# Optimization experiments

Hardware: AMD Instinct MI355X
Metric: run time of the kernel (lower is better)

## Reference

```python
import jax, jax.numpy as jnp
import numpy as np

DIM = 256
HEADS = 8
B, T, D, H, W = 2, 8, 16, 16, 16


def _mha(x, wqkv, bqkv, wo, bo):
    # x: [M, S, F]; standard self-attention (q=k=v=x), LoRA rank 0.
    M, S, F = x.shape
    hd = F // HEADS
    qkv = jnp.einsum('msf,kfg->kmsg', x, wqkv) + bqkv[:, None, None, :]  # [3,M,S,F]
    q, k, v = qkv
    q = q.reshape(M, S, HEADS, hd).transpose(0, 2, 1, 3)  # [M,Hh,S,hd]
    k = k.reshape(M, S, HEADS, hd).transpose(0, 2, 1, 3)
    v = v.reshape(M, S, HEADS, hd).transpose(0, 2, 1, 3)
    scores = jnp.einsum('mhsd,mhtd->mhst', q, k) / jnp.sqrt(jnp.asarray(hd, x.dtype))
    attn = jax.nn.softmax(scores, axis=-1)
    out = jnp.einsum('mhst,mhtd->mhsd', attn, v)
    out = out.transpose(0, 2, 1, 3).reshape(M, S, F)
    return out @ wo + bo


def _make_params(key, name_suffix):
    k1, k2 = jax.random.split(key)
    s = 1.0 / np.sqrt(DIM)
    return {
        f'wqkv_{name_suffix}': jax.random.normal(k1, (3, DIM, DIM), jnp.float32) * s,
        f'bqkv_{name_suffix}': jnp.zeros((3, DIM), jnp.float32),
        f'wo_{name_suffix}': jax.random.normal(k2, (DIM, DIM), jnp.float32) * s,
        f'bo_{name_suffix}': jnp.zeros((DIM,), jnp.float32),
    }


def setup_inputs() -> dict:
    key = jax.random.key(0)
    ks = jax.random.split(key, 5)
    inp = {'x': jax.random.normal(ks[0], (B, T, D * H * W, DIM), jnp.float32)}
    for k, ax in zip(ks[1:], ['t', 'd', 'h', 'w']):
        inp.update(_make_params(k, ax))
    inp['grid_d'] = D
    inp['grid_h'] = H
    inp['grid_w'] = W
    return inp


def reference(x, wqkv_t, bqkv_t, wo_t, bo_t,
              wqkv_d, bqkv_d, wo_d, bo_d,
              wqkv_h, bqkv_h, wo_h, bo_h,
              wqkv_w, bqkv_w, wo_w, bo_w,
              grid_d, grid_h, grid_w):
    b, t, n, f = x.shape
    d, h, w = grid_d, grid_h, grid_w
    x = x.reshape(b, t, d, h, w, f)
    if t > 1:
        xt = x.transpose(0, 2, 3, 4, 1, 5).reshape(b * d * h * w, t, f)
        xt = _mha(xt, wqkv_t, bqkv_t, wo_t, bo_t)
        xt = xt.reshape(b, d, h, w, t, f).transpose(0, 4, 1, 2, 3, 5)
        x = x + xt
    xd = x.transpose(0, 1, 3, 4, 2, 5).reshape(b * t * h * w, d, f)
    xd = _mha(xd, wqkv_d, bqkv_d, wo_d, bo_d)
    xd = xd.reshape(b, t, h, w, d, f).transpose(0, 1, 4, 2, 3, 5)
    xh = x.transpose(0, 1, 2, 4, 3, 5).reshape(b * t * d * w, h, f)
    xh = _mha(xh, wqkv_h, bqkv_h, wo_h, bo_h)
    xh = xh.reshape(b, t, d, w, h, f).transpose(0, 1, 2, 4, 3, 5)
    xw = x.reshape(b * t * d * h, w, f)
    xw = _mha(xw, wqkv_w, bqkv_w, wo_w, bo_w)
    xw = xw.reshape(b, t, d, h, w, f)
    x_comb = x + xd + xh + xw
    return x_comb.reshape(b, t, d * h * w, f)
```

## Files before the change

### kernel.cpp

```cpp
#include <hip/hip_runtime.h>

typedef __attribute__((ext_vector_type(4))) float f32x4;
typedef __attribute__((ext_vector_type(8))) short s16x8;

__device__ __forceinline__ ushort f2bf(float f) {
  union { float f; uint u; } v; v.f = f;
  uint r = v.u + 0x7fffu + ((v.u >> 16) & 1u);
  return (ushort)(r >> 16);
}

__device__ __forceinline__ void glds16(const void* g, void* l) {
  __builtin_amdgcn_global_load_lds(
      (const __attribute__((address_space(1))) uint*)g,
      (__attribute__((address_space(3))) uint*)l, 16, 0, 0);
}

__device__ __forceinline__ int asidx(int row, int col) {
  return row*256 + ((((col>>3) ^ ((row&7)<<2)))<<3) + (col&7);
}
__device__ __forceinline__ int scridx(int row, int col) {
  return row*32 + ((((col>>3) ^ ((row>>2)&3)))<<3) + (col&7);
}

struct WSrc { const float* p[8]; };

__global__ __launch_bounds__(256) void prep_weights(WSrc s, ushort* wq, ushort* wo) {
  int mm = blockIdx.x >> 6;
  int t  = blockIdx.x & 63;
  int a = mm >> 2, sub = mm & 3;
  const float* src = (sub < 3) ? (s.p[a*2] + sub*65536) : s.p[a*2+1];
  ushort*      dst = (sub < 3) ? (wq + (a*3 + sub)*65536) : (wo + a*65536);
  int gt = (t >> 3) * 32, ft = (t & 7) * 32;
  __shared__ float tile[32][33];
  int lx = threadIdx.x & 31, ly = threadIdx.x >> 5;
#pragma unroll
  for (int i = 0; i < 4; i++)
    tile[ly + i*8][lx] = src[(ft + ly + i*8)*256 + gt + lx];
  __syncthreads();
#pragma unroll
  for (int i = 0; i < 4; i++) {
    int n = gt + ly + i*8, col = ft + lx;
    dst[asidx(n, col)] = f2bf(tile[lx][ly + i*8]);
  }
}

template<int AXIS>
__device__ __forceinline__ int token_index(int blk, int row) {
  if (AXIS == 0) {
    int seq = blk*8 + (row >> 3);
    int t = row & 7;
    int b = seq >> 12, n = seq & 4095;
    return (b*8 + t)*4096 + n;
  } else {
    int sid = blk*4 + (row >> 4);
    int bt = sid >> 8, lo = sid & 255, r = row & 15;
    if (AXIS == 1) { int hh = lo >> 4, ww = lo & 15; return bt*4096 + r*256 + hh*16 + ww; }
    if (AXIS == 2) { int dd = lo >> 4, ww = lo & 15; return bt*4096 + dd*256 + r*16 + ww; }
    { int dd = lo >> 4, hh = lo & 15; return bt*4096 + dd*256 + hh*16 + r; }
  }
}

#define PUB_BARRIER() do { \
    __builtin_amdgcn_sched_barrier(0); \
    asm volatile("s_waitcnt lgkmcnt(0)" ::: "memory"); \
    __builtin_amdgcn_sched_barrier(0); \
    __builtin_amdgcn_s_barrier(); \
    __builtin_amdgcn_sched_barrier(0); } while (0)

template<int AXIS>
__global__ __launch_bounds__(512, 4) void axial_pass(
    const float* __restrict__ x0, const ushort* __restrict__ xb,
    const ushort* __restrict__ wqkvT, const float* __restrict__ bqkv,
    const ushort* __restrict__ woT, const float* __restrict__ bo,
    float* __restrict__ out, ushort* __restrict__ x1b) {

  __shared__ ushort Wbuf[2][8192];
  __shared__ ushort As[16384];
  __shared__ ushort Scr[4][2048];

  const int tid = threadIdx.x, blk = blockIdx.x;
  const int wv = tid >> 6, lane = tid & 63, llo = lane & 15, lhi = lane >> 4;
  const int pr = wv >> 1, half = wv & 1;
  const int rr = half*16 + llo;
  ushort* Qs = Scr[pr];
  ushort* Ks = Qs + 512;
  ushort* Vt = Qs + 1024;
  const f32x4 fzero = {0.f, 0.f, 0.f, 0.f};
  const s16x8 szero = {0,0,0,0,0,0,0,0};

  auto issue_stage = [&](int s) {
    const ushort* src = (s < 24) ? (wqkvT + (s % 3)*65536 + (s / 3)*8192)
                                 : (woT + (s - 24)*8192);
    const ushort* g = src + wv*1024 + lane*8;
    ushort* l = &Wbuf[s & 1][wv*1024];
    glds16(g, l);
    glds16(g + 512, l + 512);
  };

#define STAGE_SYNC(sn) do { \
    __builtin_amdgcn_sched_barrier(0); \
    asm volatile("s_waitcnt vmcnt(0) lgkmcnt(0)" ::: "memory"); \
    __builtin_amdgcn_sched_barrier(0); \
    __builtin_amdgcn_s_barrier(); \
    __builtin_amdgcn_sched_barrier(0); \
    if ((sn) < 32) issue_stage(sn); \
  } while (0)

  issue_stage(0);

  {
    int row = tid >> 3, j = tid & 7;
    int tok = token_index<AXIS>(blk, row);
    if (AXIS == 0) {
      const float4* s4 = (const float4*)(x0 + (size_t)tok*256);
#pragma unroll
      for (int i = 0; i < 4; i++) {
        int c = j + 8*i;
        float4 v0 = s4[c*2], v1 = s4[c*2 + 1];
        s16x8 o;
        o[0] = (short)f2bf(v0.x); o[1] = (short)f2bf(v0.y);
        o[2] = (short)f2bf(v0.z); o[3] = (short)f2bf(v0.w);
        o[4] = (short)f2bf(v1.x); o[5] = (short)f2bf(v1.y);
        o[6] = (short)f2bf(v1.z); o[7] = (short)f2bf(v1.w);
        *(s16x8*)(As + asidx(row, c*8)) = o;
      }
    } else {
      const s16x8* s8 = (const s16x8*)(xb + (size_t)tok*256);
#pragma unroll
      for (int i = 0; i < 4; i++) {
        int c = j + 8*i;
        *(s16x8*)(As + asidx(row, c*8)) = s8[c];
      }
    }
  }
  {
    int row = half*16 + (lane >> 2);
    int cc = 2 + (lane & 1);
    *(s16x8*)(Vt + row*32 + ((cc ^ ((row>>2)&3))<<3)) = szero;
  }
  __syncthreads();

  s16x8 af[8];
  const int xrow = pr*16 + llo;
#pragma unroll
  for (int ks = 0; ks < 8; ks++)
    af[ks] = *(const s16x8*)(As + asidx(xrow, (ks*4 + lhi)*8));

  auto proj = [&](int sb) -> f32x4 {
    const ushort* buf = Wbuf[sb];
    f32x4 c = fzero;
#pragma unroll
    for (int ks = 0; ks < 8; ks++) {
      s16x8 bv = *(const s16x8*)(buf + rr*256 + ((((ks*4+lhi) ^ ((rr&7)<<2)))<<3));
      c = __builtin_amdgcn_mfma_f32_16x16x32_bf16(af[ks], bv, c, 0, 0, 0);
    }
    return c;
  };

#pragma unroll 1
  for (int h = 0; h < 8; h++) {
    STAGE_SYNC(3*h + 1);
    {
      f32x4 c = proj((3*h) & 1);
      float bias = bqkv[0*256 + h*32 + rr];
#pragma unroll
      for (int r = 0; r < 4; r++)
        Qs[scridx(lhi*4 + r, rr)] = f2bf(c[r] + bias);
    }
    STAGE_SYNC(3*h + 2);
    {
      f32x4 c = proj((3*h + 1) & 1);
      float bias = bqkv[1*256 + h*32 + rr];
#pragma unroll
      for (int r = 0; r < 4; r++)
        Ks[scridx(lhi*4 + r, rr)] = f2bf(c[r] + bias);
    }
    STAGE_SYNC(3*h + 3);
    {
      f32x4 c = proj((3*h + 2) & 1);
      float bias = bqkv[2*256 + h*32 + rr];
#pragma unroll
      for (int r = 0; r < 4; r++)
        Vt[scridx(rr, lhi*4 + r)] = f2bf(c[r] + bias);

      s16x8 aq = *(const s16x8*)(Qs + scridx(llo, lhi*8));
      s16x8 bk = *(const s16x8*)(Ks + scridx(llo, lhi*8));
      f32x4 sc = __builtin_amdgcn_mfma_f32_16x16x32_bf16(aq, bk, fzero, 0, 0, 0);

      PUB_BARRIER();

#pragma unroll
      for (int r = 0; r < 4; r++) {
        float s = sc[r] * 0.17677669529663689f;
        if (AXIS == 0) {
          int srow = lhi*4 + r;
          if ((srow >> 3) != (llo >> 3)) s = -1e30f;
        }
        float mx = s;
        mx = fmaxf(mx, __shfl_xor(mx, 1));
        mx = fmaxf(mx, __shfl_xor(mx, 2));
        mx = fmaxf(mx, __shfl_xor(mx, 4));
        mx = fmaxf(mx, __shfl_xor(mx, 8));
        float e = __expf(s - mx);
        float sm = e;
        sm += __shfl_xor(sm, 1);
        sm += __shfl_xor(sm, 2);
        sm += __shfl_xor(sm, 4);
        sm += __shfl_xor(sm, 8);
        Ks[scridx(lhi*4 + r, llo)] = f2bf(e * __builtin_amdgcn_rcpf(sm));
      }
      s16x8 ap = *(const s16x8*)(Ks + scridx(llo, lhi*8));
      s16x8 bv = *(const s16x8*)(Vt + scridx(rr, lhi*8));
      f32x4 o = __builtin_amdgcn_mfma_f32_16x16x32_bf16(ap, bv, fzero, 0, 0, 0);
#pragma unroll
      for (int r = 0; r < 4; r++)
        As[asidx(pr*16 + lhi*4 + r, h*32 + rr)] = f2bf(o[r]);
    }
  }

  f32x4 acc[8];
#pragma unroll 1
  for (int st = 0; st < 8; st++) {
    STAGE_SYNC(25 + st);
    if (st == 0) {
#pragma unroll
      for (int ks = 0; ks < 8; ks++)
        af[ks] = *(const s16x8*)(As + asidx(xrow, (ks*4 + lhi)*8));
#pragma unroll
      for (int i = 0; i < 8; i++) acc[i] = fzero;
    }
    {
      const ushort* buf = Wbuf[st & 1];
#pragma unroll
      for (int ks = 0; ks < 8; ks++) {
        s16x8 bw = *(const s16x8*)(buf + rr*256 + ((((ks*4+lhi) ^ ((rr&7)<<2)))<<3));
        acc[st] = __builtin_amdgcn_mfma_f32_16x16x32_bf16(af[ks], bw, acc[st], 0, 0, 0);
      }
    }
  }

#pragma unroll
  for (int r = 0; r < 4; r++) {
    int row = pr*16 + lhi*4 + r;
    int tok = token_index<AXIS>(blk, row);
    size_t base = (size_t)tok*256;
#pragma unroll
    for (int st = 0; st < 8; st++) {
      int f = st*32 + half*16 + llo;
      float v = acc[st][r] + bo[f];
      if (AXIS == 0) {
        v += x0[base + f];
        out[base + f] = v;
        x1b[base + f] = f2bf(v);
      } else {
        out[base + f] += v;
      }
    }
  }
#undef STAGE_SYNC
}

extern "C" void kernel_launch(void* const* d_in, const int* in_sizes, int n_in,
                              void* d_out, int out_size, void* d_ws, size_t ws_size,
                              hipStream_t stream) {
  const float* x = (const float*)d_in[0];
  ushort* wq  = (ushort*)d_ws;
  ushort* wo  = wq + 4*3*65536;
  ushort* x1b = wo + 4*65536;
  float* out = (float*)d_out;

  WSrc wsrc;
  wsrc.p[0] = (const float*)d_in[1];  wsrc.p[1] = (const float*)d_in[3];
  wsrc.p[2] = (const float*)d_in[5];  wsrc.p[3] = (const float*)d_in[7];
  wsrc.p[4] = (const float*)d_in[9];  wsrc.p[5] = (const float*)d_in[11];
  wsrc.p[6] = (const float*)d_in[13]; wsrc.p[7] = (const float*)d_in[15];
  prep_weights<<<dim3(1024), dim3(256), 0, stream>>>(wsrc, wq, wo);

  const float* bq_t = (const float*)d_in[2];  const float* bo_t = (const float*)d_in[4];
  const float* bq_d = (const float*)d_in[6];  const float* bo_d = (const float*)d_in[8];
  const float* bq_h = (const float*)d_in[10]; const float* bo_h = (const float*)d_in[12];
  const float* bq_w = (const float*)d_in[14]; const float* bo_w = (const float*)d_in[16];

  axial_pass<0><<<dim3(1024), dim3(512), 0, stream>>>(x, nullptr, wq + 0*3*65536, bq_t, wo + 0*65536, bo_t, out, x1b);
  axial_pass<1><<<dim3(1024), dim3(512), 0, stream>>>(nullptr, x1b, wq + 1*3*65536, bq_d, wo + 1*65536, bo_d, out, nullptr);
  axial_pass<2><<<dim3(1024), dim3(512), 0, stream>>>(nullptr, x1b, wq + 2*3*65536, bq_h, wo + 2*65536, bo_h, out, nullptr);
  axial_pass<3><<<dim3(1024), dim3(512), 0, stream>>>(nullptr, x1b, wq + 3*3*65536, bq_w, wo + 3*65536, bo_w, out, nullptr);
}
```

Before: 435.8 us.

## Stage epilogue through LDS for float4 stores; split MFMA chains and change swizzle

The output epilogue now writes accumulators to a swizzled fp32 LDS tile, then each thread reads contiguous float4 chunks and does vectorized global load/add/store with bias, instead of scattered scalar accesses. The projection MFMA loops are split into two independent accumulation chains, with setprio raised around them. The As/W swizzle is changed to XOR by row&7. Shared buffers are merged into one array so the epilogue can reuse the weight region. This adds two barriers and an extra LDS round trip.

```diff
diff --git a/kernel.cpp b/kernel.cpp
--- a/kernel.cpp
+++ b/kernel.cpp
@@ -16,10 +16,13 @@
 }
 
 __device__ __forceinline__ int asidx(int row, int col) {
-  return row*256 + ((((col>>3) ^ ((row&7)<<2)))<<3) + (col&7);
+  return row*256 + ((((col>>3) ^ (row & 7)))<<3) + (col&7);
 }
 __device__ __forceinline__ int scridx(int row, int col) {
   return row*32 + ((((col>>3) ^ ((row>>2)&3)))<<3) + (col&7);
+}
+__device__ __forceinline__ int epidx(int row, int f) {
+  return row*256 + (f ^ ((row & 7) << 2));
 }
 
 struct WSrc { const float* p[8]; };
@@ -74,15 +77,17 @@
     const ushort* __restrict__ woT, const float* __restrict__ bo,
     float* __restrict__ out, ushort* __restrict__ x1b) {
 
-  __shared__ ushort Wbuf[2][8192];
-  __shared__ ushort As[16384];
-  __shared__ ushort Scr[4][2048];
+  __shared__ ushort smem[40960];
+  ushort* Wb0 = smem;
+  ushort* Wb1 = smem + 8192;
+  ushort* As  = smem + 16384;
+  ushort* ScrB = smem + 32768;
 
   const int tid = threadIdx.x, blk = blockIdx.x;
   const int wv = tid >> 6, lane = tid & 63, llo = lane & 15, lhi = lane >> 4;
   const int pr = wv >> 1, half = wv & 1;
   const int rr = half*16 + llo;
-  ushort* Qs = Scr[pr];
+  ushort* Qs = ScrB + pr*2048;
   ushort* Ks = Qs + 512;
   ushort* Vt = Qs + 1024;
   const f32x4 fzero = {0.f, 0.f, 0.f, 0.f};
@@ -92,7 +97,7 @@
     const ushort* src = (s < 24) ? (wqkvT + (s % 3)*65536 + (s / 3)*8192)
                                  : (woT + (s - 24)*8192);
     const ushort* g = src + wv*1024 + lane*8;
-    ushort* l = &Wbuf[s & 1][wv*1024];
+    ushort* l = ((s & 1) ? Wb1 : Wb0) + wv*1024;
     glds16(g, l);
     glds16(g + 512, l + 512);
   };
@@ -147,14 +152,18 @@
     af[ks] = *(const s16x8*)(As + asidx(xrow, (ks*4 + lhi)*8));
 
   auto proj = [&](int sb) -> f32x4 {
-    const ushort* buf = Wbuf[sb];
-    f32x4 c = fzero;
-#pragma unroll
-    for (int ks = 0; ks < 8; ks++) {
-      s16x8 bv = *(const s16x8*)(buf + rr*256 + ((((ks*4+lhi) ^ ((rr&7)<<2)))<<3));
-      c = __builtin_amdgcn_mfma_f32_16x16x32_bf16(af[ks], bv, c, 0, 0, 0);
-    }
-    return c;
+    const ushort* buf = sb ? Wb1 : Wb0;
+    f32x4 ca = fzero, cb = fzero;
+    __builtin_amdgcn_s_setprio(1);
+#pragma unroll
+    for (int ks = 0; ks < 4; ks++) {
+      s16x8 b0 = *(const s16x8*)(buf + asidx(rr, (ks*4 + lhi)*8));
+      s16x8 b1 = *(const s16x8*)(buf + asidx(rr, ((ks+4)*4 + lhi)*8));
+      ca = __builtin_amdgcn_mfma_f32_16x16x32_bf16(af[ks],   b0, ca, 0, 0, 0);
+      cb = __builtin_amdgcn_mfma_f32_16x16x32_bf16(af[ks+4], b1, cb, 0, 0, 0);
+    }
+    __builtin_amdgcn_s_setprio(0);
+    return ca + cb;
   };
 
 #pragma unroll 1
@@ -230,30 +239,53 @@
       for (int i = 0; i < 8; i++) acc[i] = fzero;
     }
     {
-      const ushort* buf = Wbuf[st & 1];
-#pragma unroll
-      for (int ks = 0; ks < 8; ks++) {
-        s16x8 bw = *(const s16x8*)(buf + rr*256 + ((((ks*4+lhi) ^ ((rr&7)<<2)))<<3));
-        acc[st] = __builtin_amdgcn_mfma_f32_16x16x32_bf16(af[ks], bw, acc[st], 0, 0, 0);
-      }
-    }
-  }
-
-#pragma unroll
-  for (int r = 0; r < 4; r++) {
-    int row = pr*16 + lhi*4 + r;
+      const ushort* buf = (st & 1) ? Wb1 : Wb0;
+      f32x4 t0 = fzero;
+      __builtin_amdgcn_s_setprio(1);
+#pragma unroll
+      for (int ks = 0; ks < 4; ks++) {
+        s16x8 b0 = *(const s16x8*)(buf + asidx(rr, (ks*4 + lhi)*8));
+        s16x8 b1 = *(const s16x8*)(buf + asidx(rr, ((ks+4)*4 + lhi)*8));
+        acc[st] = __builtin_amdgcn_mfma_f32_16x16x32_bf16(af[ks],   b0, acc[st], 0, 0, 0);
+        t0      = __builtin_amdgcn_mfma_f32_16x16x32_bf16(af[ks+4], b1, t0,      0, 0, 0);
+      }
+      __builtin_amdgcn_s_setprio(0);
+      acc[st] = acc[st] + t0;
+    }
+  }
+
+  float* Fep = (float*)smem;
+  PUB_BARRIER();
+#pragma unroll
+  for (int st = 0; st < 8; st++) {
+#pragma unroll
+    for (int r = 0; r < 4; r++) {
+      int row = pr*16 + lhi*4 + r;
+      Fep[epidx(row, st*32 + half*16 + llo)] = acc[st][r];
+    }
+  }
+  PUB_BARRIER();
+  {
+    int row = tid >> 3, g = tid & 7;
     int tok = token_index<AXIS>(blk, row);
     size_t base = (size_t)tok*256;
 #pragma unroll
-    for (int st = 0; st < 8; st++) {
-      int f = st*32 + half*16 + llo;
-      float v = acc[st][r] + bo[f];
+    for (int i = 0; i < 8; i++) {
+      int f = i*32 + g*4;
+      float4 v = *(float4*)&Fep[epidx(row, f)];
+      float4 b = *(const float4*)&bo[f];
+      v.x += b.x; v.y += b.y; v.z += b.z; v.w += b.w;
       if (AXIS == 0) {
-        v += x0[base + f];
-        out[base + f] = v;
-        x1b[base + f] = f2bf(v);
+        float4 x = *(const float4*)&x0[base + f];
+        v.x += x.x; v.y += x.y; v.z += x.z; v.w += x.w;
+        *(float4*)&out[base + f] = v;
+        ushort4 p; p.x = f2bf(v.x); p.y = f2bf(v.y);
+        p.z = f2bf(v.z); p.w = f2bf(v.w);
+        *(ushort4*)&x1b[base + f] = p;
       } else {
-        out[base + f] += v;
+        float4 o = *(float4*)&out[base + f];
+        o.x += v.x; o.y += v.y; o.z += v.z; o.w += v.w;
+        *(float4*)&out[base + f] = o;
       }
     }
   }
```

After: 402.8 us. 7.6% less time.

## Double rows per block and keep activations in registers across projections

Applied to the files above, without the earlier changes.

Each block now processes 128 token rows instead of 64, halving the grid, so each staged weight tile loaded into LDS feeds twice as many MFMAs. Input activations and per-head attention outputs are loaded straight into registers instead of going through a shared A tile. The epilogue stages accumulators through LDS so global reads and writes become float4-vectorised rather than scalar. It also adds s_setprio around the MFMA loops and fully unrolls the head loop, which raises register pressure and may reduce occupancy.

```diff
diff --git a/kernel.cpp b/kernel.cpp
--- a/kernel.cpp
+++ b/kernel.cpp
@@ -16,10 +16,13 @@
 }
 
 __device__ __forceinline__ int asidx(int row, int col) {
-  return row*256 + ((((col>>3) ^ ((row&7)<<2)))<<3) + (col&7);
+  return row*256 + ((((col>>3) ^ (row & 7)))<<3) + (col&7);
 }
 __device__ __forceinline__ int scridx(int row, int col) {
   return row*32 + ((((col>>3) ^ ((row>>2)&3)))<<3) + (col&7);
+}
+__device__ __forceinline__ int scrfidx(int row, int c) {
+  return row*32 + (c ^ ((row & 7) << 2));
 }
 
 struct WSrc { const float* p[8]; };
@@ -47,16 +50,16 @@
 template<int AXIS>
 __device__ __forceinline__ int token_index(int blk, int row) {
   if (AXIS == 0) {
-    int seq = blk*8 + (row >> 3);
+    int seq = blk*16 + (row >> 3);
     int t = row & 7;
     int b = seq >> 12, n = seq & 4095;
     return (b*8 + t)*4096 + n;
   } else {
-    int sid = blk*4 + (row >> 4);
+    int sid = blk*8 + (row >> 4);
     int bt = sid >> 8, lo = sid & 255, r = row & 15;
-    if (AXIS == 1) { int hh = lo >> 4, ww = lo & 15; return bt*4096 + r*256 + hh*16 + ww; }
+    if (AXIS == 1) return bt*4096 + r*256 + lo;
     if (AXIS == 2) { int dd = lo >> 4, ww = lo & 15; return bt*4096 + dd*256 + r*16 + ww; }
-    { int dd = lo >> 4, hh = lo & 15; return bt*4096 + dd*256 + hh*16 + r; }
+    return bt*4096 + lo*16 + r;
   }
 }
 
@@ -74,25 +77,22 @@
     const ushort* __restrict__ woT, const float* __restrict__ bo,
     float* __restrict__ out, ushort* __restrict__ x1b) {
 
-  __shared__ ushort Wbuf[2][8192];
-  __shared__ ushort As[16384];
-  __shared__ ushort Scr[4][2048];
+  __shared__ ushort smem[28672];
+  ushort* Wb0 = smem;
+  ushort* Wb1 = smem + 8192;
+  ushort* QKP = smem + 16384;
+  ushort* Vt  = smem + 24576;
 
   const int tid = threadIdx.x, blk = blockIdx.x;
   const int wv = tid >> 6, lane = tid & 63, llo = lane & 15, lhi = lane >> 4;
-  const int pr = wv >> 1, half = wv & 1;
-  const int rr = half*16 + llo;
-  ushort* Qs = Scr[pr];
-  ushort* Ks = Qs + 512;
-  ushort* Vt = Qs + 1024;
+  const int rg = wv >> 1, ch = wv & 1;
   const f32x4 fzero = {0.f, 0.f, 0.f, 0.f};
-  const s16x8 szero = {0,0,0,0,0,0,0,0};
 
   auto issue_stage = [&](int s) {
     const ushort* src = (s < 24) ? (wqkvT + (s % 3)*65536 + (s / 3)*8192)
                                  : (woT + (s - 24)*8192);
     const ushort* g = src + wv*1024 + lane*8;
-    ushort* l = &Wbuf[s & 1][wv*1024];
+    ushort* l = ((s & 1) ? Wb1 : Wb0) + wv*1024;
     glds16(g, l);
     glds16(g + 512, l + 512);
   };
@@ -108,152 +108,195 @@
 
   issue_stage(0);
 
-  {
-    int row = tid >> 3, j = tid & 7;
+  s16x8 af[2][8];
+#pragma unroll
+  for (int g = 0; g < 2; g++) {
+    int row = rg*32 + g*16 + llo;
     int tok = token_index<AXIS>(blk, row);
     if (AXIS == 0) {
-      const float4* s4 = (const float4*)(x0 + (size_t)tok*256);
-#pragma unroll
-      for (int i = 0; i < 4; i++) {
-        int c = j + 8*i;
-        float4 v0 = s4[c*2], v1 = s4[c*2 + 1];
+      const float* xp = x0 + (size_t)tok*256;
+#pragma unroll
+      for (int ks = 0; ks < 8; ks++) {
+        float4 a = *(const float4*)(xp + ks*32 + lhi*8);
+        float4 b = *(const float4*)(xp + ks*32 + lhi*8 + 4);
         s16x8 o;
-        o[0] = (short)f2bf(v0.x); o[1] = (short)f2bf(v0.y);
-        o[2] = (short)f2bf(v0.z); o[3] = (short)f2bf(v0.w);
-        o[4] = (short)f2bf(v1.x); o[5] = (short)f2bf(v1.y);
-        o[6] = (short)f2bf(v1.z); o[7] = (short)f2bf(v1.w);
-        *(s16x8*)(As + asidx(row, c*8)) = o;
+        o[0] = (short)f2bf(a.x); o[1] = (short)f2bf(a.y);
+        o[2] = (short)f2bf(a.z); o[3] = (short)f2bf(a.w);
+        o[4] = (short)f2bf(b.x); o[5] = (short)f2bf(b.y);
+        o[6] = (short)f2bf(b.z); o[7] = (short)f2bf(b.w);
+        af[g][ks] = o;
       }
     } else {
-      const s16x8* s8 = (const s16x8*)(xb + (size_t)tok*256);
-#pragma unroll
-      for (int i = 0; i < 4; i++) {
-        int c = j + 8*i;
-        *(s16x8*)(As + asidx(row, c*8)) = s8[c];
-      }
-    }
-  }
-  {
-    int row = half*16 + (lane >> 2);
-    int cc = 2 + (lane & 1);
-    *(s16x8*)(Vt + row*32 + ((cc ^ ((row>>2)&3))<<3)) = szero;
-  }
-  __syncthreads();
-
-  s16x8 af[8];
-  const int xrow = pr*16 + llo;
-#pragma unroll
-  for (int ks = 0; ks < 8; ks++)
-    af[ks] = *(const s16x8*)(As + asidx(xrow, (ks*4 + lhi)*8));
-
-  auto proj = [&](int sb) -> f32x4 {
-    const ushort* buf = Wbuf[sb];
-    f32x4 c = fzero;
-#pragma unroll
-    for (int ks = 0; ks < 8; ks++) {
-      s16x8 bv = *(const s16x8*)(buf + rr*256 + ((((ks*4+lhi) ^ ((rr&7)<<2)))<<3));
-      c = __builtin_amdgcn_mfma_f32_16x16x32_bf16(af[ks], bv, c, 0, 0, 0);
-    }
-    return c;
-  };
-
-#pragma unroll 1
+      const ushort* xp = xb + (size_t)tok*256;
+#pragma unroll
+      for (int ks = 0; ks < 8; ks++)
+        af[g][ks] = *(const s16x8*)(xp + ks*32 + lhi*8);
+    }
+  }
+
+  s16x8 af_o[8];
+
+#pragma unroll
   for (int h = 0; h < 8; h++) {
     STAGE_SYNC(3*h + 1);
     {
-      f32x4 c = proj((3*h) & 1);
-      float bias = bqkv[0*256 + h*32 + rr];
-#pragma unroll
-      for (int r = 0; r < 4; r++)
-        Qs[scridx(lhi*4 + r, rr)] = f2bf(c[r] + bias);
+      const ushort* buf = ((3*h) & 1) ? Wb1 : Wb0;
+      f32x4 c0 = fzero, c1 = fzero;
+      __builtin_amdgcn_s_setprio(1);
+#pragma unroll
+      for (int ks = 0; ks < 8; ks++) {
+        s16x8 bv = *(const s16x8*)(buf + asidx(ch*16 + llo, (ks*4 + lhi)*8));
+        c0 = __builtin_amdgcn_mfma_f32_16x16x32_bf16(af[0][ks], bv, c0, 0, 0, 0);
+        c1 = __builtin_amdgcn_mfma_f32_16x16x32_bf16(af[1][ks], bv, c1, 0, 0, 0);
+      }
+      __builtin_amdgcn_s_setprio(0);
+      float bi = bqkv[h*32 + ch*16 + llo];
+      ushort* q0 = QKP + (rg*2 + 0)*1024;
+      ushort* q1 = QKP + (rg*2 + 1)*1024;
+#pragma unroll
+      for (int r = 0; r < 4; r++) {
+        q0[scridx(lhi*4 + r, ch*16 + llo)] = f2bf(c0[r] + bi);
+        q1[scridx(lhi*4 + r, ch*16 + llo)] = f2bf(c1[r] + bi);
+      }
     }
     STAGE_SYNC(3*h + 2);
     {
-      f32x4 c = proj((3*h + 1) & 1);
-      float bias = bqkv[1*256 + h*32 + rr];
-#pragma unroll
-      for (int r = 0; r < 4; r++)
-        Ks[scridx(lhi*4 + r, rr)] = f2bf(c[r] + bias);
+      const ushort* buf = ((3*h + 1) & 1) ? Wb1 : Wb0;
+      f32x4 c0 = fzero, c1 = fzero;
+      __builtin_amdgcn_s_setprio(1);
+#pragma unroll
+      for (int ks = 0; ks < 8; ks++) {
+        s16x8 bv = *(const s16x8*)(buf + asidx(ch*16 + llo, (ks*4 + lhi)*8));
+        c0 = __builtin_amdgcn_mfma_f32_16x16x32_bf16(af[0][ks], bv, c0, 0, 0, 0);
+        c1 = __builtin_amdgcn_mfma_f32_16x16x32_bf16(af[1][ks], bv, c1, 0, 0, 0);
+      }
+      __builtin_amdgcn_s_setprio(0);
+      float bi = bqkv[256 + h*32 + ch*16 + llo];
+      ushort* k0 = QKP + (rg*2 + 0)*1024 + 512;
+      ushort* k1 = QKP + (rg*2 + 1)*1024 + 512;
+#pragma unroll
+      for (int r = 0; r < 4; r++) {
+        k0[scridx(lhi*4 + r, ch*16 + llo)] = f2bf(c0[r] + bi);
+        k1[scridx(lhi*4 + r, ch*16 + llo)] = f2bf(c1[r] + bi);
+      }
     }
     STAGE_SYNC(3*h + 3);
     {
-      f32x4 c = proj((3*h + 2) & 1);
-      float bias = bqkv[2*256 + h*32 + rr];
-#pragma unroll
-      for (int r = 0; r < 4; r++)
-        Vt[scridx(rr, lhi*4 + r)] = f2bf(c[r] + bias);
-
-      s16x8 aq = *(const s16x8*)(Qs + scridx(llo, lhi*8));
-      s16x8 bk = *(const s16x8*)(Ks + scridx(llo, lhi*8));
+      const ushort* buf = ((3*h + 2) & 1) ? Wb1 : Wb0;
+      f32x4 c0 = fzero, c1 = fzero;
+      __builtin_amdgcn_s_setprio(1);
+#pragma unroll
+      for (int ks = 0; ks < 8; ks++) {
+        s16x8 bv = *(const s16x8*)(buf + asidx(ch*16 + llo, (ks*4 + lhi)*8));
+        c0 = __builtin_amdgcn_mfma_f32_16x16x32_bf16(af[0][ks], bv, c0, 0, 0, 0);
+        c1 = __builtin_amdgcn_mfma_f32_16x16x32_bf16(af[1][ks], bv, c1, 0, 0, 0);
+      }
+      __builtin_amdgcn_s_setprio(0);
+      float bi = bqkv[512 + h*32 + ch*16 + llo];
+      ushort* vt = Vt + rg*1024;
+#pragma unroll
+      for (int r = 0; r < 4; r++) {
+        vt[scridx(ch*16 + llo, 0*16 + lhi*4 + r)] = f2bf(c0[r] + bi);
+        vt[scridx(ch*16 + llo, 1*16 + lhi*4 + r)] = f2bf(c1[r] + bi);
+      }
+    }
+    PUB_BARRIER();
+
+    {
+      ushort* myQ  = QKP + wv*1024;
+      ushort* myKP = myQ + 512;
+      const ushort* myVt = Vt + (wv >> 1)*1024;
+      const int mh = wv & 1;
+      s16x8 aq = *(const s16x8*)(myQ  + scridx(llo, lhi*8));
+      s16x8 bk = *(const s16x8*)(myKP + scridx(llo, lhi*8));
       f32x4 sc = __builtin_amdgcn_mfma_f32_16x16x32_bf16(aq, bk, fzero, 0, 0, 0);
-
-      PUB_BARRIER();
-
-#pragma unroll
-      for (int r = 0; r < 4; r++) {
-        float s = sc[r] * 0.17677669529663689f;
+#pragma unroll
+      for (int r = 0; r < 4; r++) {
+        float sv = sc[r] * 0.17677669529663689f;
         if (AXIS == 0) {
           int srow = lhi*4 + r;
-          if ((srow >> 3) != (llo >> 3)) s = -1e30f;
+          if ((srow >> 3) != (llo >> 3)) sv = -1e30f;
         }
-        float mx = s;
+        float mx = sv;
         mx = fmaxf(mx, __shfl_xor(mx, 1));
         mx = fmaxf(mx, __shfl_xor(mx, 2));
         mx = fmaxf(mx, __shfl_xor(mx, 4));
         mx = fmaxf(mx, __shfl_xor(mx, 8));
-        float e = __expf(s - mx);
+        float e = __expf(sv - mx);
         float sm = e;
         sm += __shfl_xor(sm, 1);
         sm += __shfl_xor(sm, 2);
         sm += __shfl_xor(sm, 4);
         sm += __shfl_xor(sm, 8);
-        Ks[scridx(lhi*4 + r, llo)] = f2bf(e * __builtin_amdgcn_rcpf(sm));
-      }
-      s16x8 ap = *(const s16x8*)(Ks + scridx(llo, lhi*8));
-      s16x8 bv = *(const s16x8*)(Vt + scridx(rr, lhi*8));
-      f32x4 o = __builtin_amdgcn_mfma_f32_16x16x32_bf16(ap, bv, fzero, 0, 0, 0);
-#pragma unroll
-      for (int r = 0; r < 4; r++)
-        As[asidx(pr*16 + lhi*4 + r, h*32 + rr)] = f2bf(o[r]);
-    }
-  }
-
-  f32x4 acc[8];
+        myKP[scridx(lhi*4 + r, mh*16 + llo)]       = f2bf(e * __builtin_amdgcn_rcpf(sm));
+        myKP[scridx(lhi*4 + r, (1 - mh)*16 + llo)] = 0;
+      }
+      s16x8 ap  = *(const s16x8*)(myKP + scridx(llo, lhi*8));
+      s16x8 bv0 = *(const s16x8*)(myVt + scridx(llo, lhi*8));
+      s16x8 bv1 = *(const s16x8*)(myVt + scridx(16 + llo, lhi*8));
+      f32x4 o0 = __builtin_amdgcn_mfma_f32_16x16x32_bf16(ap, bv0, fzero, 0, 0, 0);
+      f32x4 o1 = __builtin_amdgcn_mfma_f32_16x16x32_bf16(ap, bv1, fzero, 0, 0, 0);
+#pragma unroll
+      for (int r = 0; r < 4; r++) {
+        myQ[scridx(lhi*4 + r, llo)]      = f2bf(o0[r]);
+        myQ[scridx(lhi*4 + r, 16 + llo)] = f2bf(o1[r]);
+      }
+      af_o[h] = *(const s16x8*)(myQ + scridx(llo, lhi*8));
+    }
+  }
+
 #pragma unroll 1
   for (int st = 0; st < 8; st++) {
     STAGE_SYNC(25 + st);
-    if (st == 0) {
-#pragma unroll
-      for (int ks = 0; ks < 8; ks++)
-        af[ks] = *(const s16x8*)(As + asidx(xrow, (ks*4 + lhi)*8));
-#pragma unroll
-      for (int i = 0; i < 8; i++) acc[i] = fzero;
-    }
-    {
-      const ushort* buf = Wbuf[st & 1];
-#pragma unroll
-      for (int ks = 0; ks < 8; ks++) {
-        s16x8 bw = *(const s16x8*)(buf + rr*256 + ((((ks*4+lhi) ^ ((rr&7)<<2)))<<3));
-        acc[st] = __builtin_amdgcn_mfma_f32_16x16x32_bf16(af[ks], bw, acc[st], 0, 0, 0);
-      }
-    }
-  }
-
-#pragma unroll
-  for (int r = 0; r < 4; r++) {
-    int row = pr*16 + lhi*4 + r;
-    int tok = token_index<AXIS>(blk, row);
-    size_t base = (size_t)tok*256;
-#pragma unroll
-    for (int st = 0; st < 8; st++) {
-      int f = st*32 + half*16 + llo;
-      float v = acc[st][r] + bo[f];
+    const ushort* buf = (st & 1) ? Wb1 : Wb0;
+    f32x4 c0 = fzero, c1 = fzero;
+    __builtin_amdgcn_s_setprio(1);
+#pragma unroll
+    for (int ks = 0; ks < 8; ks++) {
+      s16x8 b0 = *(const s16x8*)(buf + asidx(llo,      (ks*4 + lhi)*8));
+      s16x8 b1 = *(const s16x8*)(buf + asidx(16 + llo, (ks*4 + lhi)*8));
+      c0 = __builtin_amdgcn_mfma_f32_16x16x32_bf16(af_o[ks], b0, c0, 0, 0, 0);
+      c1 = __builtin_amdgcn_mfma_f32_16x16x32_bf16(af_o[ks], b1, c1, 0, 0, 0);
+    }
+    __builtin_amdgcn_s_setprio(0);
+
+    float* Scf = (float*)(QKP + wv*1024);
+#pragma unroll
+    for (int r = 0; r < 4; r++) {
+      Scf[scrfidx(lhi*4 + r, llo)]      = c0[r];
+      Scf[scrfidx(lhi*4 + r, 16 + llo)] = c1[r];
+    }
+    {
+      int row = lane >> 2, cb = (lane & 3)*8;
+      float4 fa = *(const float4*)&Scf[scrfidx(row, cb)];
+      float4 fb = *(const float4*)&Scf[scrfidx(row, cb + 4)];
+      int col = st*32 + cb;
+      int tok = token_index<AXIS>(blk, wv*16 + row);
+      size_t base = (size_t)tok*256;
+      float4 ba = *(const float4*)&bo[col];
+      float4 bb4 = *(const float4*)&bo[col + 4];
+      fa.x += ba.x; fa.y += ba.y; fa.z += ba.z; fa.w += ba.w;
+      fb.x += bb4.x; fb.y += bb4.y; fb.z += bb4.z; fb.w += bb4.w;
       if (AXIS == 0) {
-        v += x0[base + f];
-        out[base + f] = v;
-        x1b[base + f] = f2bf(v);
+        float4 xa = *(const float4*)&x0[base + col];
+        float4 xb4 = *(const float4*)&x0[base + col + 4];
+        fa.x += xa.x; fa.y += xa.y; fa.z += xa.z; fa.w += xa.w;
+        fb.x += xb4.x; fb.y += xb4.y; fb.z += xb4.z; fb.w += xb4.w;
+        *(float4*)&out[base + col]     = fa;
+        *(float4*)&out[base + col + 4] = fb;
+        s16x8 p;
+        p[0] = (short)f2bf(fa.x); p[1] = (short)f2bf(fa.y);
+        p[2] = (short)f2bf(fa.z); p[3] = (short)f2bf(fa.w);
+        p[4] = (short)f2bf(fb.x); p[5] = (short)f2bf(fb.y);
+        p[6] = (short)f2bf(fb.z); p[7] = (short)f2bf(fb.w);
+        *(s16x8*)&x1b[base + col] = p;
       } else {
-        out[base + f] += v;
+        float4 oa = *(float4*)&out[base + col];
+        float4 ob = *(float4*)&out[base + col + 4];
+        oa.x += fa.x; oa.y += fa.y; oa.z += fa.z; oa.w += fa.w;
+        ob.x += fb.x; ob.y += fb.y; ob.z += fb.z; ob.w += fb.w;
+        *(float4*)&out[base + col]     = oa;
+        *(float4*)&out[base + col + 4] = ob;
       }
     }
   }
@@ -281,8 +324,8 @@
   const float* bq_h = (const float*)d_in[10]; const float* bo_h = (const float*)d_in[12];
   const float* bq_w = (const float*)d_in[14]; const float* bo_w = (const float*)d_in[16];
 
-  axial_pass<0><<<dim3(1024), dim3(512), 0, stream>>>(x, nullptr, wq + 0*3*65536, bq_t, wo + 0*65536, bo_t, out, x1b);
-  axial_pass<1><<<dim3(1024), dim3(512), 0, stream>>>(nullptr, x1b, wq + 1*3*65536, bq_d, wo + 1*65536, bo_d, out, nullptr);
-  axial_pass<2><<<dim3(1024), dim3(512), 0, stream>>>(nullptr, x1b, wq + 2*3*65536, bq_h, wo + 2*65536, bo_h, out, nullptr);
-  axial_pass<3><<<dim3(1024), dim3(512), 0, stream>>>(nullptr, x1b, wq + 3*3*65536, bq_w, wo + 3*65536, bo_w, out, nullptr);
-}
+  axial_pass<0><<<dim3(512), dim3(512), 0, stream>>>(x, nullptr, wq + 0*3*65536, bq_t, wo + 0*65536, bo_t, out, x1b);
+  axial_pass<1><<<dim3(512), dim3(512), 0, stream>>>(nullptr, x1b, wq + 1*3*65536, bq_d, wo + 1*65536, bo_d, out, nullptr);
+  axial_pass<2><<<dim3(512), dim3(512), 0, stream>>>(nullptr, x1b, wq + 2*3*65536, bq_h, wo + 2*65536, bo_h, out, nullptr);
+  axial_pass<3><<<dim3(512), dim3(512), 0, stream>>>(nullptr, x1b, wq + 3*3*65536, bq_w, wo + 3*65536, bo_w, out, nullptr);
+}
```

After: 521.9 us. 1.2x slower.
